# Kernel tuning notes

Hardware: AMD Instinct MI355X
Metric: run time of the kernel (lower is better)

Reference implementation:

```python
import jax, jax.numpy as jnp
import numpy as np

N, IN_DIM, OUT_DIM, HEADS = 4096, 128, 32, 4
EDGE_PROB = 0.015  # ~61 neighbors/node on average


def setup_inputs() -> dict:
    key = jax.random.key(0)
    k1, k2, k3, k4 = jax.random.split(key, 4)
    x = jax.random.normal(k1, (N, IN_DIM), dtype=jnp.float32)
    adj = (jax.random.uniform(k2, (N, N)) < EDGE_PROB).astype(jnp.float32)
    adj = jnp.maximum(adj, jnp.eye(N, dtype=jnp.float32))  # self loops so softmax is never all-masked
    # nn.Linear(in_dim, out_dim*heads, bias=False): weight stored here as [in, out]
    W = jax.random.normal(k3, (IN_DIM, OUT_DIM * HEADS), dtype=jnp.float32) / np.sqrt(IN_DIM).astype(np.float32)
    # nn.Linear(2*out_dim, 1, bias=False) -> a single [2*out_dim] vector shared across heads
    a = jax.random.normal(k4, (2 * OUT_DIM,), dtype=jnp.float32) / np.sqrt(2 * OUT_DIM).astype(np.float32)
    return {"x": x, "adj": adj, "W": W, "a": a}


def reference(x, adj, W, a):
    n = x.shape[0]
    xp = (x @ W).reshape(n, HEADS, OUT_DIM)  # [N, H, D]
    # Original builds concat([x_expanded, x_j_expanded])[i,j] = [x[j] || x[i]] and applies
    # a linear map. Since attn is linear, scores decompose: e[i,j,h] = a1.x[j,h] + a2.x[i,h].
    a_j, a_i = a[:OUT_DIM], a[OUT_DIM:]
    s_j = jnp.einsum('nhd,d->nh', xp, a_j)  # contribution of column node j
    s_i = jnp.einsum('nhd,d->nh', xp, a_i)  # contribution of row node i
    scale = jnp.float32(1.0 / np.sqrt(OUT_DIM))
    e = (s_i[:, None, :] + s_j[None, :, :]) * scale  # [N, N, H]
    e = e + ((1.0 - adj) * jnp.float32(-1e9))[:, :, None]
    att = jax.nn.softmax(e, axis=1)  # softmax over dim=1 (neighbors j), as in original
    out = jnp.einsum('ijh,jhd->ihd', att, xp)  # attention-weighted neighbor aggregation
    return out.reshape(n, HEADS * OUT_DIM)
```

## Files before the change

### kernel.cpp

```cpp
#include <hip/hip_runtime.h>

#define N_NODES 4096
#define IN_DIM  128
#define OUT_DIM 32
#define HEADS   4
#define FDIM    128
#define K1_ROWS 8
#define CAP     192

static __device__ __forceinline__ unsigned bf16pack(float a, float b) {
    unsigned ua = __float_as_uint(a), ub = __float_as_uint(b);
    ua = (ua + 0x7FFFu + ((ua >> 16) & 1u)) >> 16;
    ub = (ub + 0x7FFFu + ((ub >> 16) & 1u)) >> 16;
    return ua | (ub << 16);
}

__global__ __launch_bounds__(256) void gat_proj(const float* __restrict__ x,
                                                const float* __restrict__ W,
                                                const float* __restrict__ a,
                                                unsigned* __restrict__ Ybf,
                                                float* __restrict__ Eg) {
    __shared__ float xs[K1_ROWS * IN_DIM];
    __shared__ float eS[K1_ROWS][HEADS];
    const int t    = threadIdx.x;
    const int row0 = blockIdx.x * K1_ROWS;

    ((float4*)xs)[t] = ((const float4*)(x + (size_t)row0 * IN_DIM))[t];
    __syncthreads();

    const int c  = t & 127;
    const int rg = t >> 7;
    const float* xb = xs + (rg * 4) * IN_DIM;

    float acc0 = 0.f, acc1 = 0.f, acc2 = 0.f, acc3 = 0.f;
#pragma unroll 4
    for (int k0 = 0; k0 < IN_DIM; k0 += 4) {
        const float w0 = W[(k0 + 0) * FDIM + c];
        const float w1 = W[(k0 + 1) * FDIM + c];
        const float w2 = W[(k0 + 2) * FDIM + c];
        const float w3 = W[(k0 + 3) * FDIM + c];
        const float4 x0 = *(const float4*)(xb + 0 * IN_DIM + k0);
        const float4 x1 = *(const float4*)(xb + 1 * IN_DIM + k0);
        const float4 x2 = *(const float4*)(xb + 2 * IN_DIM + k0);
        const float4 x3 = *(const float4*)(xb + 3 * IN_DIM + k0);
        acc0 = fmaf(x0.x, w0, fmaf(x0.y, w1, fmaf(x0.z, w2, fmaf(x0.w, w3, acc0))));
        acc1 = fmaf(x1.x, w0, fmaf(x1.y, w1, fmaf(x1.z, w2, fmaf(x1.w, w3, acc1))));
        acc2 = fmaf(x2.x, w0, fmaf(x2.y, w1, fmaf(x2.z, w2, fmaf(x2.w, w3, acc2))));
        acc3 = fmaf(x3.x, w0, fmaf(x3.y, w1, fmaf(x3.z, w2, fmaf(x3.w, w3, acc3))));
    }

    const int rb = rg * 4;
    __syncthreads();
    xs[(rb + 0) * FDIM + c] = acc0;
    xs[(rb + 1) * FDIM + c] = acc1;
    xs[(rb + 2) * FDIM + c] = acc2;
    xs[(rb + 3) * FDIM + c] = acc3;
    __syncthreads();

    if (t < K1_ROWS * HEADS) {
        const int r = t >> 2, h = t & 3;
        const float4* xr = (const float4*)(xs + r * FDIM + h * OUT_DIM);
        const float4* aj = (const float4*)a;
        float vj = 0.f;
#pragma unroll
        for (int q = 0; q < 8; ++q) {
            const float4 xv = xr[q], a0 = aj[q];
            vj += xv.x * a0.x + xv.y * a0.y + xv.z * a0.z + xv.w * a0.w;
        }
        const float e = __expf(vj * 0.17677669529663687f);
        eS[r][h] = e;
        Eg[(row0 + r) * HEADS + h] = e;
    }
    __syncthreads();

#pragma unroll
    for (int q = 0; q < 2; ++q) {
        const int idx = t + 256 * q;
        const int r   = idx >> 6;
        const int cp  = idx & 63;
        const float e = eS[r][cp >> 4];
        const float a0 = xs[r * FDIM + 2 * cp]     * e;
        const float a1 = xs[r * FDIM + 2 * cp + 1] * e;
        Ybf[(size_t)(row0 + r) * 64 + cp] = bf16pack(a0, a1);
    }
}

__global__ __launch_bounds__(256, 8) void gat_sum(const float* __restrict__ adj,
                                                  const unsigned* __restrict__ Ybf,
                                                  const float* __restrict__ E,
                                                  float* __restrict__ out) {
    const int tid  = threadIdx.x;
    const int wv   = tid >> 6;
    const int lane = tid & 63;
    const int row  = blockIdx.x * 2 + (wv >> 1);
    const int half = wv & 1;
    const int g    = lane >> 4;
    const int q    = lane & 15;
    const int head = q >> 2;

    __shared__ int   seg_s[4][CAP + 16];
    __shared__ float part[4][16][12];

    const float4* arow = (const float4*)(adj + (size_t)row * N_NODES) + half * 512;
    const unsigned long long lt = (1ULL << lane) - 1ULL;
    int* seg = seg_s[wv];

    int cnt;
    {
        float4 v[8];
#pragma unroll
        for (int c = 0; c < 8; ++c) v[c] = arow[c * 64 + lane];

        int base = 0;
#pragma unroll
        for (int c = 0; c < 8; ++c) {
            const int cb = half * 2048 + c * 256 + lane * 4;
            const float vals[4] = {v[c].x, v[c].y, v[c].z, v[c].w};
#pragma unroll
            for (int m = 0; m < 4; ++m) {
                const unsigned long long mk = __ballot(vals[m] != 0.f);
                const int pos = base + __popcll(mk & lt);
                if (vals[m] != 0.f && pos < CAP) seg[pos] = cb + m;
                base += __popcll(mk);
            }
        }
        cnt = base;
    }

    const uint4* Yv = (const uint4*)Ybf;
    float a0 = 0.f, a1 = 0.f, a2 = 0.f, a3 = 0.f;
    float a4 = 0.f, a5 = 0.f, a6 = 0.f, a7 = 0.f, z = 0.f;

#define ACC(u, ev)                                                            \
    {                                                                         \
        a0 += __uint_as_float((u).x << 16);                                   \
        a1 += __uint_as_float((u).x & 0xFFFF0000u);                           \
        a2 += __uint_as_float((u).y << 16);                                   \
        a3 += __uint_as_float((u).y & 0xFFFF0000u);                           \
        a4 += __uint_as_float((u).z << 16);                                   \
        a5 += __uint_as_float((u).z & 0xFFFF0000u);                           \
        a6 += __uint_as_float((u).w << 16);                                   \
        a7 += __uint_as_float((u).w & 0xFFFF0000u);                           \
        z  += (ev);                                                           \
    }

    if (__builtin_expect(cnt <= CAP, 1)) {
        int p = 0;
        for (; p + 16 <= cnt; p += 16) {
            const int4 jq = *(const int4*)&seg[p + 4 * g];
            const uint4 y0 = Yv[(size_t)jq.x * 16 + q];
            const uint4 y1 = Yv[(size_t)jq.y * 16 + q];
            const uint4 y2 = Yv[(size_t)jq.z * 16 + q];
            const uint4 y3 = Yv[(size_t)jq.w * 16 + q];
            const float e0 = E[(size_t)jq.x * 4 + head];
            const float e1 = E[(size_t)jq.y * 4 + head];
            const float e2 = E[(size_t)jq.z * 4 + head];
            const float e3 = E[(size_t)jq.w * 4 + head];
            ACC(y0, e0) ACC(y1, e1) ACC(y2, e2) ACC(y3, e3)
        }
        if (p < cnt) {
            const int eb = p + 4 * g;
            const int4 jq = *(const int4*)&seg[eb];
            const bool k0 = eb + 0 < cnt, k1 = eb + 1 < cnt;
            const bool k2 = eb + 2 < cnt, k3 = eb + 3 < cnt;
            const int j0 = k0 ? jq.x : 0, j1 = k1 ? jq.y : 0;
            const int j2 = k2 ? jq.z : 0, j3 = k3 ? jq.w : 0;
            const uint4 y0 = Yv[(size_t)j0 * 16 + q];
            const uint4 y1 = Yv[(size_t)j1 * 16 + q];
            const uint4 y2 = Yv[(size_t)j2 * 16 + q];
            const uint4 y3 = Yv[(size_t)j3 * 16 + q];
            const float e0 = E[(size_t)j0 * 4 + head];
            const float e1 = E[(size_t)j1 * 4 + head];
            const float e2 = E[(size_t)j2 * 4 + head];
            const float e3 = E[(size_t)j3 * 4 + head];
            if (k0) ACC(y0, e0)
            if (k1) ACC(y1, e1)
            if (k2) ACC(y2, e2)
            if (k3) ACC(y3, e3)
        }
    } else {
        int ep = 0;
        for (int c = 0; c < 8; ++c) {
            const float4 vv = arow[c * 64 + lane];
            const float vals[4] = {vv.x, vv.y, vv.z, vv.w};
#pragma unroll
            for (int m = 0; m < 4; ++m) {
                unsigned long long mask = __ballot(vals[m] != 0.f);
                while (mask) {
                    const int b = __builtin_ctzll(mask);
                    mask &= mask - 1ULL;
                    if ((ep & 3) == g) {
                        const int j = half * 2048 + c * 256 + b * 4 + m;
                        const uint4 y = Yv[(size_t)j * 16 + q];
                        const float e = E[(size_t)j * 4 + head];
                        ACC(y, e)
                    }
                    ++ep;
                }
            }
        }
    }
#undef ACC

#pragma unroll
    for (int off = 16; off < 64; off <<= 1) {
        a0 += __shfl_xor(a0, off);
        a1 += __shfl_xor(a1, off);
        a2 += __shfl_xor(a2, off);
        a3 += __shfl_xor(a3, off);
        a4 += __shfl_xor(a4, off);
        a5 += __shfl_xor(a5, off);
        a6 += __shfl_xor(a6, off);
        a7 += __shfl_xor(a7, off);
        z  += __shfl_xor(z, off);
    }

    if (lane < 16) {
        float* pr = part[wv][q];
        pr[0] = a0; pr[1] = a1; pr[2] = a2; pr[3] = a3;
        pr[4] = a4; pr[5] = a5; pr[6] = a6; pr[7] = a7;
        pr[8] = z;
    }
    __syncthreads();

    if ((wv & 1) == 0 && lane < 16) {
        const float* pa = part[wv][q];
        const float* pb = part[wv + 1][q];
        const float invZ = 1.0f / (pa[8] + pb[8]);
        float4 o0, o1;
        o0.x = (pa[0] + pb[0]) * invZ;
        o0.y = (pa[1] + pb[1]) * invZ;
        o0.z = (pa[2] + pb[2]) * invZ;
        o0.w = (pa[3] + pb[3]) * invZ;
        o1.x = (pa[4] + pb[4]) * invZ;
        o1.y = (pa[5] + pb[5]) * invZ;
        o1.z = (pa[6] + pb[6]) * invZ;
        o1.w = (pa[7] + pb[7]) * invZ;
        float4* orow = (float4*)(out + (size_t)row * FDIM + q * 8);
        orow[0] = o0;
        orow[1] = o1;
    }
}

extern "C" void kernel_launch(void* const* d_in, const int* in_sizes, int n_in,
                              void* d_out, int out_size, void* d_ws, size_t ws_size,
                              hipStream_t stream) {
    const float* x   = (const float*)d_in[0];
    const float* adj = (const float*)d_in[1];
    const float* W   = (const float*)d_in[2];
    const float* a   = (const float*)d_in[3];
    float* out = (float*)d_out;

    unsigned* Ybf = (unsigned*)d_ws;
    float*    E   = (float*)(Ybf + (size_t)N_NODES * 64);

    gat_proj<<<N_NODES / K1_ROWS, 256, 0, stream>>>(x, W, a, Ybf, E);
    gat_sum<<<N_NODES / 2, 256, 0, stream>>>(adj, Ybf, E, out);
}
```

Baseline: 27.84 us.

## Pack adjacency into bitmasks in a merged prep kernel, one wave per row

The adjacency scan moves out of the aggregation kernel into a combined prep kernel. Its extra blocks turn the dense float matrix into 64-bit ballot bitmasks, running alongside the projection blocks. The sum kernel then reads 512 bytes of bits per row instead of 16KB of floats, and it assigns one wave per row. That removes the cross-wave LDS reduction and __syncthreads. The 64MB adjacency read still happens once, but it now overlaps with projection, at the cost of a bitmask write/read round trip and a serial prefix scan.

```diff
diff --git a/kernel.cpp b/kernel.cpp
--- a/kernel.cpp
+++ b/kernel.cpp
@@ -6,7 +6,9 @@
 #define HEADS   4
 #define FDIM    128
 #define K1_ROWS 8
-#define CAP     192
+#define CAP     256
+#define NBITSBLK 2048
+#define NPROJBLK (N_NODES / K1_ROWS)
 
 static __device__ __forceinline__ unsigned bf16pack(float a, float b) {
     unsigned ua = __float_as_uint(a), ub = __float_as_uint(b);
@@ -15,15 +17,42 @@
     return ua | (ub << 16);
 }
 
-__global__ __launch_bounds__(256) void gat_proj(const float* __restrict__ x,
-                                                const float* __restrict__ W,
-                                                const float* __restrict__ a,
-                                                unsigned* __restrict__ Ybf,
-                                                float* __restrict__ Eg) {
+__global__ __launch_bounds__(256, 8) void gat_prep(const float* __restrict__ adj,
+                                                   const float* __restrict__ x,
+                                                   const float* __restrict__ W,
+                                                   const float* __restrict__ a,
+                                                   unsigned long long* __restrict__ bits,
+                                                   unsigned* __restrict__ Ybf,
+                                                   float* __restrict__ Eg) {
+    if (blockIdx.x < NBITSBLK) {
+        const int wv   = threadIdx.x >> 6;
+        const int lane = threadIdx.x & 63;
+        const size_t wj = (size_t)blockIdx.x * 4 + wv;
+        const float4* A4 = (const float4*)adj;
+
+        float4 v[8];
+#pragma unroll
+        for (int it = 0; it < 8; ++it)
+            v[it] = A4[(wj * 8 + it) * 64 + lane];
+
+#pragma unroll
+        for (int it = 0; it < 8; ++it) {
+            const unsigned long long m0 = __ballot(v[it].x != 0.f);
+            const unsigned long long m1 = __ballot(v[it].y != 0.f);
+            const unsigned long long m2 = __ballot(v[it].z != 0.f);
+            const unsigned long long m3 = __ballot(v[it].w != 0.f);
+            if (lane == 0) {
+                unsigned long long* p = bits + (wj * 8 + it) * 4;
+                p[0] = m0; p[1] = m1; p[2] = m2; p[3] = m3;
+            }
+        }
+        return;
+    }
+
     __shared__ float xs[K1_ROWS * IN_DIM];
     __shared__ float eS[K1_ROWS][HEADS];
     const int t    = threadIdx.x;
-    const int row0 = blockIdx.x * K1_ROWS;
+    const int row0 = (blockIdx.x - NBITSBLK) * K1_ROWS;
 
     ((float4*)xs)[t] = ((const float4*)(x + (size_t)row0 * IN_DIM))[t];
     __syncthreads();
@@ -85,46 +114,39 @@
     }
 }
 
-__global__ __launch_bounds__(256, 8) void gat_sum(const float* __restrict__ adj,
+__global__ __launch_bounds__(256, 8) void gat_sum(const unsigned long long* __restrict__ bits,
                                                   const unsigned* __restrict__ Ybf,
                                                   const float* __restrict__ E,
                                                   float* __restrict__ out) {
-    const int tid  = threadIdx.x;
-    const int wv   = tid >> 6;
-    const int lane = tid & 63;
-    const int row  = blockIdx.x * 2 + (wv >> 1);
-    const int half = wv & 1;
+    const int wv   = threadIdx.x >> 6;
+    const int lane = threadIdx.x & 63;
+    const int row  = blockIdx.x * 4 + wv;
     const int g    = lane >> 4;
     const int q    = lane & 15;
     const int head = q >> 2;
 
-    __shared__ int   seg_s[4][CAP + 16];
-    __shared__ float part[4][16][12];
-
-    const float4* arow = (const float4*)(adj + (size_t)row * N_NODES) + half * 512;
-    const unsigned long long lt = (1ULL << lane) - 1ULL;
+    __shared__ int seg_s[4][CAP + 16];
     int* seg = seg_s[wv];
 
-    int cnt;
+    const unsigned long long w64 = bits[(size_t)row * 64 + lane];
+    const int pc = __popcll(w64);
+    int inc = pc;
+#pragma unroll
+    for (int d = 1; d < 64; d <<= 1) {
+        const int tt = __shfl_up(inc, d);
+        if (lane >= d) inc += tt;
+    }
+    const int cnt = __shfl(inc, 63);
     {
-        float4 v[8];
-#pragma unroll
-        for (int c = 0; c < 8; ++c) v[c] = arow[c * 64 + lane];
-
-        int base = 0;
-#pragma unroll
-        for (int c = 0; c < 8; ++c) {
-            const int cb = half * 2048 + c * 256 + lane * 4;
-            const float vals[4] = {v[c].x, v[c].y, v[c].z, v[c].w};
-#pragma unroll
-            for (int m = 0; m < 4; ++m) {
-                const unsigned long long mk = __ballot(vals[m] != 0.f);
-                const int pos = base + __popcll(mk & lt);
-                if (vals[m] != 0.f && pos < CAP) seg[pos] = cb + m;
-                base += __popcll(mk);
-            }
-        }
-        cnt = base;
+        int p = inc - pc;
+        unsigned long long m = w64;
+        const int cb = (lane >> 2) * 256 + (lane & 3);
+        while (m) {
+            const int b = __builtin_ctzll(m);
+            m &= m - 1ULL;
+            if (p < CAP) seg[p] = cb + b * 4;
+            ++p;
+        }
     }
 
     const uint4* Yv = (const uint4*)Ybf;
@@ -180,23 +202,19 @@
         }
     } else {
         int ep = 0;
-        for (int c = 0; c < 8; ++c) {
-            const float4 vv = arow[c * 64 + lane];
-            const float vals[4] = {vv.x, vv.y, vv.z, vv.w};
-#pragma unroll
-            for (int m = 0; m < 4; ++m) {
-                unsigned long long mask = __ballot(vals[m] != 0.f);
-                while (mask) {
-                    const int b = __builtin_ctzll(mask);
-                    mask &= mask - 1ULL;
-                    if ((ep & 3) == g) {
-                        const int j = half * 2048 + c * 256 + b * 4 + m;
-                        const uint4 y = Yv[(size_t)j * 16 + q];
-                        const float e = E[(size_t)j * 4 + head];
-                        ACC(y, e)
-                    }
-                    ++ep;
+        for (int k = 0; k < 64; ++k) {
+            unsigned long long m = __shfl(w64, k);
+            const int cbk = (k >> 2) * 256 + (k & 3);
+            while (m) {
+                const int b = __builtin_ctzll(m);
+                m &= m - 1ULL;
+                if ((ep & 3) == g) {
+                    const int j = cbk + b * 4;
+                    const uint4 y = Yv[(size_t)j * 16 + q];
+                    const float e = E[(size_t)j * 4 + head];
+                    ACC(y, e)
                 }
+                ++ep;
             }
         }
     }
@@ -216,26 +234,10 @@
     }
 
     if (lane < 16) {
-        float* pr = part[wv][q];
-        pr[0] = a0; pr[1] = a1; pr[2] = a2; pr[3] = a3;
-        pr[4] = a4; pr[5] = a5; pr[6] = a6; pr[7] = a7;
-        pr[8] = z;
-    }
-    __syncthreads();
-
-    if ((wv & 1) == 0 && lane < 16) {
-        const float* pa = part[wv][q];
-        const float* pb = part[wv + 1][q];
-        const float invZ = 1.0f / (pa[8] + pb[8]);
+        const float invZ = 1.0f / z;
         float4 o0, o1;
-        o0.x = (pa[0] + pb[0]) * invZ;
-        o0.y = (pa[1] + pb[1]) * invZ;
-        o0.z = (pa[2] + pb[2]) * invZ;
-        o0.w = (pa[3] + pb[3]) * invZ;
-        o1.x = (pa[4] + pb[4]) * invZ;
-        o1.y = (pa[5] + pb[5]) * invZ;
-        o1.z = (pa[6] + pb[6]) * invZ;
-        o1.w = (pa[7] + pb[7]) * invZ;
+        o0.x = a0 * invZ; o0.y = a1 * invZ; o0.z = a2 * invZ; o0.w = a3 * invZ;
+        o1.x = a4 * invZ; o1.y = a5 * invZ; o1.z = a6 * invZ; o1.w = a7 * invZ;
         float4* orow = (float4*)(out + (size_t)row * FDIM + q * 8);
         orow[0] = o0;
         orow[1] = o1;
@@ -253,7 +255,9 @@
 
     unsigned* Ybf = (unsigned*)d_ws;
     float*    E   = (float*)(Ybf + (size_t)N_NODES * 64);
-
-    gat_proj<<<N_NODES / K1_ROWS, 256, 0, stream>>>(x, W, a, Ybf, E);
-    gat_sum<<<N_NODES / 2, 256, 0, stream>>>(adj, Ybf, E, out);
-}
+    unsigned long long* bits =
+        (unsigned long long*)(E + (size_t)N_NODES * HEADS);
+
+    gat_prep<<<NBITSBLK + NPROJBLK, 256, 0, stream>>>(adj, x, W, a, bits, Ybf, E);
+    gat_sum<<<N_NODES / 4, 256, 0, stream>>>(bits, Ybf, E, out);
+}
```

Measured after the change: 29.35 us. 5.4% more time.
